# Performance work log

Measured on AMD Instinct MI355X. Metric: run time of the kernel, lower is better.

## Reference

```python
import jax, jax.numpy as jnp
from jax import lax
import numpy as np

K = 3          # k_size
STRIDE = 1
LAMDA = 10.0
B, H, W_, D = 2, 64, 64, 64


def extract_patches(x, k, stride, same):
    """TF tf.image.extract_patches layout: per-position vector ordered (ki, kj, channel)."""
    b, h, w, d = x.shape
    kn = (k - 1) // 2
    if same:  # SAME padding, stride 1 (as used for fg patches)
        x = jnp.pad(x, ((0, 0), (kn, kn), (kn, kn), (0, 0)))
        ph, pw = h, w
    else:     # VALID with stride
        ph = (h - k) // stride + 1
        pw = (w - k) // stride + 1
    cols = [x[:, i:i + (ph - 1) * stride + 1:stride, j:j + (pw - 1) * stride + 1:stride, :]
            for i in range(k) for j in range(k)]
    return jnp.stack(cols, axis=3).reshape(b, ph, pw, k * k * d)


def setup_inputs() -> dict:
    key = jax.random.key(0)
    k1, k2, k3, k4 = jax.random.split(key, 4)
    bg_in = jax.random.normal(k1, (B, H, W_, D), jnp.float32)
    fg_in = jax.random.normal(k2, (B, H, W_, D), jnp.float32)
    m = (jax.random.uniform(k3, (B, H, W_, 1)) > 0.3).astype(jnp.float32)
    mask = jnp.broadcast_to(m, (B, H, W_, D)) + jnp.zeros((), jnp.float32)
    W_ml = jax.random.normal(k4, (2 * D, D), jnp.float32) * 0.05  # 1x1 conv 'ML'
    b_ml = jnp.zeros((D,), jnp.float32)
    return {"bg_in": bg_in, "fg_in": fg_in, "mask": mask, "W_ml": W_ml, "b_ml": b_ml}


def reference(bg_in, fg_in, mask, W_ml, b_ml):
    b, h, w, d = bg_in.shape
    kn = (K - 1) // 2
    # nearest resize to (h,w) is identity here; take channel 0, tile to d channels
    mask_r = jnp.broadcast_to(mask[..., :1], (b, h, w, d))
    bg = bg_in * mask_r
    ph = (h - K) // STRIDE + 1
    pw = (w - K) // STRIDE + 1
    c = ph * pw
    # background patches: (b, c, k*k*d); foreground patches: (b, h, w, k*k*d)
    patch1 = extract_patches(bg, K, STRIDE, False).reshape(b, c, K * K * d)
    patch2 = extract_patches(fg_in, K, 1, True)
    k1d = jnp.sum(patch1 * patch1, axis=2)          # (b, c)
    wwd = jnp.sum(patch2 * patch2, axis=3)          # (b, h, w)
    # 1x1 conv of fg patches against bg patch bank == cross-correlation
    CS = jnp.einsum('bhwp,bcp->bhwc', patch2, patch1)
    DS1 = k1d[:, None, None, :] + wwd[..., None] - 2.0 * CS   # squared distances (b,h,w,c)
    mu = jnp.mean(DS1, axis=-1, keepdims=True)
    sd = jnp.std(DS1, axis=-1, keepdims=True)       # population std, as tf.math.reduce_std
    DS2 = -jnp.tanh((DS1 - mu) / sd)
    # exp(x-3)/sum(exp(x-3)) == softmax(x)
    CA = jax.nn.softmax(LAMDA * DS2, axis=-1)       # (b, h, w, c)
    # per-sample transposed conv with bg patches as kernel (k2: (b,K,K,d,c))
    k2 = patch1.reshape(b, c, K, K, d).transpose(0, 2, 3, 4, 1)
    # tf.nn.conv2d_transpose == gradient of SAME conv: correlate with rot180 kernel, swap I/O
    kt = k2[:, ::-1, ::-1].transpose(0, 1, 2, 4, 3)  # (b, K, K, c, d)

    def tconv(ca, ker):
        return lax.conv_general_dilated(ca[None], ker, (1, 1), 'SAME',
                                        dimension_numbers=('NHWC', 'HWIO', 'NHWC'))[0]

    ACL = jax.vmap(tconv)(CA, kt) / float(K * K)    # (b, h, w, d)
    ACL = bg + ACL * (1.0 - mask_r)
    con1 = jnp.concatenate([bg_in, ACL], axis=-1)   # (b, h, w, 2d)
    out = jax.nn.elu(jnp.einsum('bhwc,co->bhwo', con1, W_ml) + b_ml)
    return out
```

## Files before the change

kernel.cpp:

```cpp
#include <hip/hip_runtime.h>
#include <hip/hip_fp16.h>
#include <math.h>

#define BB 2
#define HH 64
#define WW 64
#define DD 64
#define PH 62
#define CC 3844
#define CCP 3968
#define PL 576
#define PLP 640
#define TP 8
#define LAM 10.0f

typedef _Float16 f16;
typedef __attribute__((ext_vector_type(8))) _Float16 half8;
typedef __attribute__((ext_vector_type(4))) float f32x4;

#define REQ_FAST 90030080ULL

__device__ __forceinline__ void gld16(const void* g, void* l) {
  __builtin_amdgcn_global_load_lds((const __attribute__((address_space(1))) void*)g,
                                   (__attribute__((address_space(3))) void*)l, 16, 0, 0);
}

__global__ __launch_bounds__(256) void k_prep2(
    const float* __restrict__ bg_in, const float* __restrict__ fg,
    const float* __restrict__ mask, float* __restrict__ bg,
    f16* __restrict__ bgf, f16* __restrict__ fgp) {
  const int NBG = BB * 4288 * 64;
  const int NFG = BB * 4356 * 64;
  int idx = blockIdx.x * 256 + threadIdx.x;
  if (idx < NBG) {
    int ch = idx & 63;
    int pix = (idx >> 6) % 4288;
    int b = idx / (4288 * 64);
    if (pix < 4096) {
      size_t src = ((size_t)b * 4096 + pix) * 64 + ch;
      float v = bg_in[src] * mask[((size_t)b * 4096 + pix) * 64];
      bg[src] = v;
      bgf[idx] = (f16)v;
    } else {
      bgf[idx] = (f16)0.f;
    }
  } else if (idx < NBG + NFG) {
    int i2 = idx - NBG;
    int ch = i2 & 63;
    int pix = (i2 >> 6) % 4356;
    int b = i2 / (4356 * 64);
    int yy = pix / 66, xx = pix - 66 * yy;
    float v = 0.f;
    if (yy >= 1 && yy <= 64 && xx >= 1 && xx <= 64)
      v = fg[(((size_t)b * 64 + (yy - 1)) * 64 + (xx - 1)) * 64 + ch];
    fgp[i2] = (f16)v;
  }
}

__global__ __launch_bounds__(256) void k_p1t(const float* __restrict__ bg,
                                             f16* __restrict__ P1T) {
  int idx = blockIdx.x * 256 + threadIdx.x;
  if (idx >= BB * PLP * CCP) return;
  int c = idx % CCP;
  int rest = idx / CCP;
  int r = rest % PLP, b = rest / PLP;
  float v = 0.f;
  if (r < PL && c < CC) {
    int ci = c / PH, cj = c - ci * PH;
    int kk = r >> 6, ch = r & 63;
    int ki = kk / 3, kj = kk - 3 * ki;
    v = bg[(((size_t)b * HH + ci + ki) * WW + cj + kj) * DD + ch];
  }
  P1T[idx] = (f16)v;
}

__global__ __launch_bounds__(256) void k_k1d2(const float* __restrict__ bg,
                                              float* __restrict__ k1d) {
  int idx = blockIdx.x * 256 + threadIdx.x;
  if (idx >= BB * CC) return;
  int b = idx / CC, c = idx - b * CC;
  int ci = c / PH, cj = c - ci * PH;
  float s = 0.f;
  for (int ki = 0; ki < 3; ++ki)
    for (int kj = 0; kj < 3; ++kj) {
      const float4* p =
          (const float4*)(bg + (((size_t)(b * HH + ci + ki) * WW) + cj + kj) * DD);
#pragma unroll
      for (int q = 0; q < 16; ++q) {
        float4 v = p[q];
        s += v.x * v.x + v.y * v.y + v.z * v.z + v.w * v.w;
      }
    }
  k1d[(size_t)b * CCP + c] = s;
}

__global__ __launch_bounds__(512) void k_gemm1(
    const f16* __restrict__ fgp, const f16* __restrict__ bgf,
    f16* __restrict__ CS) {
  __shared__ f16 tA[2][128 * 64];
  __shared__ f16 tB[2][128 * 64];
  const int tid = threadIdx.x;
  const int l = tid & 63, w = tid >> 6;
  const int b = blockIdx.z;
  const int m0 = blockIdx.y * 128, n0 = blockIdx.x * 128;
  const f16* fgB = fgp + (size_t)b * (4356 * 64);
  const f16* bgB = bgf + (size_t)b * (4288 * 64);

  int pixA[2], chSA[2], aCh[2];
#pragma unroll
  for (int i = 0; i < 2; ++i) {
    aCh[i] = w * 2 + i;
    int li = aCh[i] * 64 + l;
    int r = li >> 3;
    int j = (li & 7) ^ (r & 7);
    chSA[i] = j * 8;
    int pos = m0 + r;
    pixA[i] = (pos >> 6) * 66 + (pos & 63);
  }
  int pixB[2], chSB[2], bCh[2];
#pragma unroll
  for (int i = 0; i < 2; ++i) {
    bCh[i] = w * 2 + i;
    int li = bCh[i] * 64 + l;
    int r = li >> 3;
    int j = (li & 7) ^ (r & 7);
    chSB[i] = j * 8;
    int c = n0 + r;
    if (c < CC) {
      int ci = c / 62;
      pixB[i] = ci * 64 + (c - 62 * ci);
    } else {
      pixB[i] = 4096;
    }
  }

  const int wm = (w >> 2) * 64, wn = (w & 3) * 32;
  const int lr = l & 15, lk = l >> 4;
  const int xr = (lr & 7) << 4;

  f32x4 acc[4][2];
#pragma unroll
  for (int mi = 0; mi < 4; ++mi)
#pragma unroll
    for (int ni = 0; ni < 2; ++ni) acc[mi][ni] = (f32x4){0.f, 0.f, 0.f, 0.f};

#pragma unroll
  for (int i = 0; i < 2; ++i) {
    gld16(fgB + (size_t)pixA[i] * 64 + chSA[i], (char*)tA[0] + aCh[i] * 1024);
    gld16(bgB + (size_t)pixB[i] * 64 + chSB[i], (char*)tB[0] + bCh[i] * 1024);
  }
  asm volatile("s_waitcnt vmcnt(0)" ::: "memory");
  __syncthreads();

#pragma unroll 1
  for (int t = 0; t < 9; ++t) {
    const int cur = t & 1;
    if (t + 1 < 9) {
      const int tn = t + 1;
      const int ki = tn / 3, kj = tn - 3 * ki;
      const int offA = ki * 66 + kj, offB = ki * 64 + kj;
#pragma unroll
      for (int i = 0; i < 2; ++i) {
        gld16(fgB + (size_t)(pixA[i] + offA) * 64 + chSA[i],
              (char*)tA[cur ^ 1] + aCh[i] * 1024);
        gld16(bgB + (size_t)(pixB[i] + offB) * 64 + chSB[i],
              (char*)tB[cur ^ 1] + bCh[i] * 1024);
      }
    }
#pragma unroll
    for (int kk = 0; kk < 2; ++kk) {
      half8 av[4], bv[2];
      const int cb = lk * 16 + kk * 64;
#pragma unroll
      for (int mi = 0; mi < 4; ++mi) {
        int r = wm + mi * 16 + lr;
        av[mi] = *(const half8*)((const char*)tA[cur] + r * 128 + (cb ^ xr));
      }
#pragma unroll
      for (int ni = 0; ni < 2; ++ni) {
        int r = wn + ni * 16 + lr;
        bv[ni] = *(const half8*)((const char*)tB[cur] + r * 128 + (cb ^ xr));
      }
#pragma unroll
      for (int mi = 0; mi < 4; ++mi)
#pragma unroll
        for (int ni = 0; ni < 2; ++ni)
          acc[mi][ni] = __builtin_amdgcn_mfma_f32_16x16x32_f16(
              av[mi], bv[ni], acc[mi][ni], 0, 0, 0);
    }
    asm volatile("s_waitcnt vmcnt(0)" ::: "memory");
    __syncthreads();
  }

  CS += (size_t)b * 4096 * CCP;
#pragma unroll
  for (int mi = 0; mi < 4; ++mi) {
#pragma unroll
    for (int q = 0; q < 4; ++q) {
      int m = m0 + wm + mi * 16 + lk * 4 + q;
#pragma unroll
      for (int ni = 0; ni < 2; ++ni) {
        int n = n0 + wn + ni * 16 + lr;
        CS[(size_t)m * CCP + n] = (f16)acc[mi][ni][q];
      }
    }
  }
}

__global__ __launch_bounds__(512) void k_gemm2(
    const f16* __restrict__ A, const f16* __restrict__ B, f16* __restrict__ C,
    const float* __restrict__ sden) {
  __shared__ f16 tA[2][64 * 64];
  __shared__ f16 tB[2][128 * 64];
  const int tid = threadIdx.x;
  const int l = tid & 63, w = tid >> 6;
  const int p = blockIdx.x;
  const int L = (p & 7) * 80 + (p >> 3);
  const int b = L / 320;
  const int rL = L - b * 320;
  const int mt = rL / 5, nt = rL - mt * 5;
  const int m0 = mt * 64, n0 = nt * 128;
  A += (size_t)b * 4096 * CCP;
  B += (size_t)b * PLP * CCP;
  C += (size_t)b * 4096 * PLP;
  const float* sd = sden + (size_t)b * 4096;

  size_t aOff;
  {
    int li = w * 64 + l;
    int r = li >> 3;
    int j = (li & 7) ^ (r & 7);
    aOff = (size_t)(m0 + r) * CCP + j * 8;
  }
  size_t bOff[2];
  int bCh[2];
#pragma unroll
  for (int i = 0; i < 2; ++i) {
    bCh[i] = w * 2 + i;
    int li = bCh[i] * 64 + l;
    int r = li >> 3;
    int j = (li & 7) ^ (r & 7);
    bOff[i] = (size_t)(n0 + r) * CCP + j * 8;
  }

  const int wm = (w >> 2) * 32, wn = (w & 3) * 32;
  const int lr = l & 15, lk = l >> 4;
  const int xr = (lr & 7) << 4;

  f32x4 acc[2][2];
#pragma unroll
  for (int mi = 0; mi < 2; ++mi)
#pragma unroll
    for (int ni = 0; ni < 2; ++ni) acc[mi][ni] = (f32x4){0.f, 0.f, 0.f, 0.f};

  auto STAGE = [&](int buf, int k0) {
    gld16(A + aOff + k0, (char*)tA[buf] + w * 1024);
#pragma unroll
    for (int i = 0; i < 2; ++i)
      gld16(B + bOff[i] + k0, (char*)tB[buf] + bCh[i] * 1024);
  };

  const int NT = CCP / 64;
  STAGE(0, 0);
  asm volatile("s_waitcnt vmcnt(0)" ::: "memory");
  __syncthreads();

#pragma unroll 1
  for (int t = 0; t < NT; ++t) {
    const int cur = t & 1;
    if (t + 1 < NT) STAGE(cur ^ 1, (t + 1) * 64);
#pragma unroll
    for (int kk = 0; kk < 2; ++kk) {
      half8 av[2], bv[2];
      const int cb = lk * 16 + kk * 64;
#pragma unroll
      for (int mi = 0; mi < 2; ++mi) {
        int r = wm + mi * 16 + lr;
        av[mi] = *(const half8*)((const char*)tA[cur] + r * 128 + (cb ^ xr));
      }
#pragma unroll
      for (int ni = 0; ni < 2; ++ni) {
        int r = wn + ni * 16 + lr;
        bv[ni] = *(const half8*)((const char*)tB[cur] + r * 128 + (cb ^ xr));
      }
#pragma unroll
      for (int mi = 0; mi < 2; ++mi)
#pragma unroll
        for (int ni = 0; ni < 2; ++ni)
          acc[mi][ni] = __builtin_amdgcn_mfma_f32_16x16x32_f16(
              av[mi], bv[ni], acc[mi][ni], 0, 0, 0);
    }
    asm volatile("s_waitcnt vmcnt(0)" ::: "memory");
    __syncthreads();
  }

#pragma unroll
  for (int mi = 0; mi < 2; ++mi) {
#pragma unroll
    for (int q = 0; q < 4; ++q) {
      int m = m0 + wm + mi * 16 + lk * 4 + q;
      float sc = sd[m];
#pragma unroll
      for (int ni = 0; ni < 2; ++ni) {
        int n = n0 + wn + ni * 16 + lr;
        C[(size_t)m * PLP + n] = (f16)(acc[mi][ni][q] * sc);
      }
    }
  }
}

__global__ __launch_bounds__(256) void k_stats(f16* __restrict__ CS,
                                               const float* __restrict__ k1d,
                                               float* __restrict__ sden) {
  __shared__ float red[8];
  const int tid = threadIdx.x;
  const int row = blockIdx.x, b = blockIdx.y;
  f16* cs = CS + ((size_t)b * 4096 + row) * CCP;
  const float* kd = k1d + (size_t)b * CCP;
  const int base = tid * 16;
  const bool act = base < CCP;

  float tv[16];
  float s1 = 0.f, s2 = 0.f;
  if (act) {
    half8 v0 = ((const half8*)(cs + base))[0];
    half8 v1 = ((const half8*)(cs + base))[1];
    float kv[16];
    *(float4*)(kv + 0) = ((const float4*)(kd + base))[0];
    *(float4*)(kv + 4) = ((const float4*)(kd + base))[1];
    *(float4*)(kv + 8) = ((const float4*)(kd + base))[2];
    *(float4*)(kv + 12) = ((const float4*)(kd + base))[3];
#pragma unroll
    for (int i = 0; i < 16; ++i) {
      float cval = (float)(i < 8 ? v0[i] : v1[i - 8]);
      float t = (base + i < CC) ? (kv[i] - 2.f * cval) : 0.f;
      tv[i] = t;
      s1 += t;
      s2 = fmaf(t, t, s2);
    }
  } else {
#pragma unroll
    for (int i = 0; i < 16; ++i) tv[i] = 0.f;
  }
#pragma unroll
  for (int m = 32; m; m >>= 1) {
    s1 += __shfl_xor(s1, m, 64);
    s2 += __shfl_xor(s2, m, 64);
  }
  if ((tid & 63) == 0) {
    red[tid >> 6] = s1;
    red[4 + (tid >> 6)] = s2;
  }
  __syncthreads();
  float mu = (red[0] + red[1] + red[2] + red[3]) * (1.f / CC);
  float ex2 = (red[4] + red[5] + red[6] + red[7]) * (1.f / CC);
  float var = fmaxf(ex2 - mu * mu, 1e-12f);
  float rsd = rsqrtf(var);
  __syncthreads();

  float den = 0.f;
  if (act) {
    half8 w0, w1;
#pragma unroll
    for (int i = 0; i < 16; ++i) {
      float wv = 0.f;
      if (base + i < CC) {
        float z = (tv[i] - mu) * rsd;
        float e2z = __expf(2.f * z);
        float th = 1.f - 2.f / (e2z + 1.f);
        wv = __expf(-LAM * th);
        den += wv;
      }
      if (i < 8) w0[i] = (f16)wv; else w1[i - 8] = (f16)wv;
    }
    ((half8*)(cs + base))[0] = w0;
    ((half8*)(cs + base))[1] = w1;
  }
#pragma unroll
  for (int m = 32; m; m >>= 1) den += __shfl_xor(den, m, 64);
  if ((tid & 63) == 0) red[tid >> 6] = den;
  __syncthreads();
  if (tid == 0)
    sden[(size_t)b * 4096 + row] = 1.f / (9.f * (red[0] + red[1] + red[2] + red[3]));
}

__global__ __launch_bounds__(256) void k_final2(
    const float* __restrict__ bg_in, const float* __restrict__ mask,
    const float* __restrict__ bg, const f16* __restrict__ N2,
    const float* __restrict__ Wml, const float* __restrict__ bml,
    float* __restrict__ out) {
  __shared__ float s_con[4 * 128];
  const int tid = threadIdx.x;
  const int posg = blockIdx.x * 4;
  for (int i = tid; i < 4 * 128; i += 256) {
    int p = i >> 7, c = i & 127;
    int pos = posg + p;
    float v;
    if (c < 64) {
      v = bg_in[(size_t)pos * DD + c];
    } else {
      int cc = c - 64;
      int bwx = pos & 4095, bb = pos >> 12;
      int y = bwx >> 6, x = bwx & 63;
      float a = 0.f;
#pragma unroll
      for (int s = 0; s < 3; ++s) {
        int yy = y + 1 - s;
        if (yy < 0 || yy >= HH) continue;
#pragma unroll
        for (int t = 0; t < 3; ++t) {
          int xx = x + 1 - t;
          if (xx < 0 || xx >= WW) continue;
          a += (float)N2[((size_t)bb * 4096 + yy * 64 + xx) * PLP + (s * 3 + t) * 64 + cc];
        }
      }
      float m0 = mask[(size_t)pos * DD];
      v = bg[(size_t)pos * DD + cc] + a * (1.f - m0);
    }
    s_con[i] = v;
  }
  __syncthreads();
  const int o = tid & 63, p = tid >> 6;
  float sum = bml[o];
  const float* cp = s_con + (p << 7);
#pragma unroll 8
  for (int c = 0; c < 128; ++c) sum = fmaf(cp[c], Wml[c * 64 + o], sum);
  out[(size_t)(posg + p) * 64 + o] = (sum > 0.f) ? sum : expm1f(sum);
}

#define WS_BG    0
#define WS_BGT   524288
#define WS_K1D   1048576
#define WS_ACLN  1056264

__global__ __launch_bounds__(256) void k_prep(
    const float* __restrict__ bg_in, const float* __restrict__ mask,
    float* __restrict__ bg, float* __restrict__ bgT) {
  int idx = blockIdx.x * 256 + threadIdx.x;
  if (idx >= BB * HH * WW * DD) return;
  int ch = idx & 63, pos = idx >> 6;
  float m = mask[(size_t)pos * DD];
  float v = bg_in[idx] * m;
  bg[idx] = v;
  int x = pos & 63, rest = pos >> 6;
  int y = rest & 63, b = rest >> 6;
  bgT[(((size_t)b * DD + ch) * HH + y) * WW + x] = v;
}

__global__ __launch_bounds__(256) void k_k1d(const float* __restrict__ bg,
                                             float* __restrict__ k1d) {
  int idx = blockIdx.x * 256 + threadIdx.x;
  if (idx >= BB * CC) return;
  int b = idx / CC, c = idx - b * CC;
  int ci = c / PH, cj = c - ci * PH;
  float s = 0.f;
  for (int ki = 0; ki < 3; ++ki)
    for (int kj = 0; kj < 3; ++kj) {
      const float4* p =
          (const float4*)(bg + (((size_t)(b * HH + ci + ki) * WW) + cj + kj) * DD);
#pragma unroll
      for (int q = 0; q < 16; ++q) {
        float4 v = p[q];
        s += v.x * v.x + v.y * v.y + v.z * v.z + v.w * v.w;
      }
    }
  k1d[idx] = s;
}

__global__ __launch_bounds__(256, 2) void k_heavy(
    const float* __restrict__ fg, const float* __restrict__ bg,
    const float* __restrict__ bgT, const float* __restrict__ k1d,
    float* __restrict__ acln) {
  __shared__ _Float16 s_cs[TP * CC];
  __shared__ float s_fg[TP * PL];
  __shared__ float s_red[8];
  __shared__ float s_wwd[TP];
  __shared__ float s_den[TP];

  const int tid = threadIdx.x;
  const int X0 = blockIdx.x * TP;
  const int Y = blockIdx.y;
  const int b = blockIdx.z;

  for (int i = tid; i < TP * PL; i += 256) {
    int p = i / PL, r = i - p * PL;
    int kk = r >> 6, ch = r & 63;
    int ki = kk / 3, kj = kk - 3 * ki;
    int hy = Y + ki - 1, wx = X0 + p + kj - 1;
    float v = 0.f;
    if (hy >= 0 && hy < HH && wx >= 0 && wx < WW)
      v = fg[(((size_t)b * HH + hy) * WW + wx) * DD + ch];
    s_fg[i] = v;
  }
  __syncthreads();
  {
    int p = tid >> 5, lane = tid & 31;
    float a = 0.f;
    for (int r = lane; r < PL; r += 32) {
      float v = s_fg[p * PL + r];
      a = fmaf(v, v, a);
    }
#pragma unroll
    for (int m = 16; m; m >>= 1) a += __shfl_xor(a, m, 64);
    if (lane == 0) s_wwd[p] = a;
  }
  __syncthreads();

  const float* bgTb = bgT + (size_t)b * DD * HH * WW;
  for (int sw = 0; sw < 4; ++sw) {
    const int cb = sw * 256 + tid;
    float acc[TP][4];
#pragma unroll
    for (int p = 0; p < TP; ++p)
#pragma unroll
      for (int q = 0; q < 4; ++q) acc[p][q] = 0.f;
    int off4[4];
#pragma unroll
    for (int q = 0; q < 4; ++q) {
      int c = cb + q * 1024;
      if (c >= CC) c = CC - 1;
      int ci = c / PH;
      off4[q] = ci * WW + (c - ci * PH);
    }
    for (int ch = 0; ch < DD; ++ch) {
      const float* bgTc = bgTb + (size_t)ch * (HH * WW);
#pragma unroll
      for (int kk = 0; kk < 9; ++kk) {
        const int ki = kk / 3, kj = kk - 3 * (kk / 3);
        float fv[TP];
#pragma unroll
        for (int p = 0; p < TP; ++p) fv[p] = s_fg[p * PL + (kk << 6) + ch];
        float bv[4];
#pragma unroll
        for (int q = 0; q < 4; ++q) bv[q] = bgTc[off4[q] + ki * WW + kj];
#pragma unroll
        for (int p = 0; p < TP; ++p)
#pragma unroll
          for (int q = 0; q < 4; ++q) acc[p][q] = fmaf(fv[p], bv[q], acc[p][q]);
      }
    }
#pragma unroll
    for (int q = 0; q < 4; ++q) {
      int c = cb + q * 1024;
      if (c < CC) {
#pragma unroll
        for (int p = 0; p < TP; ++p) s_cs[p * CC + c] = (_Float16)acc[p][q];
      }
    }
  }
  __syncthreads();

  const float* k1db = k1d + b * CC;
  for (int pos = 0; pos < TP; ++pos) {
    __syncthreads();
    const float wwdp = s_wwd[pos];
    float s1 = 0.f, s2 = 0.f;
    for (int c = tid; c < CC; c += 256) {
      float ds1 = k1db[c] + wwdp - 2.f * (float)s_cs[pos * CC + c];
      s1 += ds1;
      s2 = fmaf(ds1, ds1, s2);
    }
#pragma unroll
    for (int m = 32; m; m >>= 1) {
      s1 += __shfl_xor(s1, m, 64);
      s2 += __shfl_xor(s2, m, 64);
    }
    if ((tid & 63) == 0) {
      int w = tid >> 6;
      s_red[w] = s1;
      s_red[4 + w] = s2;
    }
    __syncthreads();
    float mu = (s_red[0] + s_red[1] + s_red[2] + s_red[3]) * (1.f / CC);
    float ex2 = (s_red[4] + s_red[5] + s_red[6] + s_red[7]) * (1.f / CC);
    float var = fmaxf(ex2 - mu * mu, 1e-12f);
    float rsd = rsqrtf(var);
    float dp = 0.f;
    for (int c = tid; c < CC; c += 256) {
      float ds1 = k1db[c] + wwdp - 2.f * (float)s_cs[pos * CC + c];
      float z = (ds1 - mu) * rsd;
      float wv = expf(-LAM * tanhf(z));
      s_cs[pos * CC + c] = (_Float16)wv;
      dp += wv;
    }
#pragma unroll
    for (int m = 32; m; m >>= 1) dp += __shfl_xor(dp, m, 64);
    __syncthreads();
    if ((tid & 63) == 0) s_red[tid >> 6] = dp;
    __syncthreads();
    if (tid == 0) s_den[pos] = s_red[0] + s_red[1] + s_red[2] + s_red[3];
  }

  const int d = tid & 63;
  const int grp = tid >> 6;
  const int oA = grp, oB = grp + 4;
  const int sA = oA / 3, tA = oA - 3 * sA;
  const int sB = oB / 3, tB = oB - 3 * sB;
  const bool hasC = (grp == 0);
  const int offA = (sA * WW + tA) * DD + d;
  const int offB = (sB * WW + tB) * DD + d;
  const int offC = (2 * WW + 2) * DD + d;
  float aA[TP], aB[TP], aC[TP];
#pragma unroll
  for (int p = 0; p < TP; ++p) { aA[p] = 0.f; aB[p] = 0.f; aC[p] = 0.f; }
  const float* bgb = bg + (size_t)b * HH * WW * DD;
  float* s_wf = s_fg;
  int cj = 0, rowoff = 0;
  for (int c0 = 0; c0 < CC; c0 += 128) {
    const int n = (CC - c0 < 128) ? (CC - c0) : 128;
    __syncthreads();
    for (int i = tid; i < TP * 128; i += 256) {
      int p = i >> 7, cc = i & 127;
      s_wf[i] = (cc < n) ? (float)s_cs[p * CC + c0 + cc] : 0.f;
    }
    __syncthreads();
    for (int cc = 0; cc < n; cc += 2) {
      float2 wv[TP];
#pragma unroll
      for (int p = 0; p < TP; ++p)
        wv[p] = *(const float2*)(s_wf + (p << 7) + cc);
      {
        const float* rp = bgb + (size_t)rowoff * DD;
        float bA = rp[offA], bB = rp[offB], bCv = rp[offC];
#pragma unroll
        for (int p = 0; p < TP; ++p) {
          aA[p] = fmaf(wv[p].x, bA, aA[p]);
          aB[p] = fmaf(wv[p].x, bB, aB[p]);
          if (hasC) aC[p] = fmaf(wv[p].x, bCv, aC[p]);
        }
        ++rowoff;
        if (++cj == PH) { cj = 0; rowoff += 2; }
      }
      {
        const float* rp = bgb + (size_t)rowoff * DD;
        float bA = rp[offA], bB = rp[offB], bCv = rp[offC];
#pragma unroll
        for (int p = 0; p < TP; ++p) {
          aA[p] = fmaf(wv[p].y, bA, aA[p]);
          aB[p] = fmaf(wv[p].y, bB, aB[p]);
          if (hasC) aC[p] = fmaf(wv[p].y, bCv, aC[p]);
        }
        ++rowoff;
        if (++cj == PH) { cj = 0; rowoff += 2; }
      }
    }
  }
  __syncthreads();
#pragma unroll
  for (int p = 0; p < TP; ++p) {
    const float inv = 1.f / (9.f * s_den[p]);
    float* dst = acln + ((((size_t)b * HH + Y) * WW + (X0 + p)) * 9) * 64;
    dst[oA * 64 + d] = aA[p] * inv;
    dst[oB * 64 + d] = aB[p] * inv;
    if (hasC) dst[512 + d] = aC[p] * inv;
  }
}

__global__ __launch_bounds__(256) void k_final(
    const float* __restrict__ bg_in, const float* __restrict__ mask,
    const float* __restrict__ bg, const float* __restrict__ acln,
    const float* __restrict__ Wml, const float* __restrict__ bml,
    float* __restrict__ out) {
  __shared__ float s_con[4 * 128];
  const int tid = threadIdx.x;
  const int posg = blockIdx.x * 4;
  for (int i = tid; i < 4 * 128; i += 256) {
    int p = i >> 7, c = i & 127;
    int pos = posg + p;
    float v;
    if (c < 64) {
      v = bg_in[(size_t)pos * DD + c];
    } else {
      int cc = c - 64;
      int bwx = pos & 4095, bb = pos >> 12;
      int y = bwx >> 6, x = bwx & 63;
      float a = 0.f;
#pragma unroll
      for (int s = 0; s < 3; ++s) {
        int yy = y + 1 - s;
        if (yy < 0 || yy >= HH) continue;
#pragma unroll
        for (int t = 0; t < 3; ++t) {
          int xx = x + 1 - t;
          if (xx < 0 || xx >= WW) continue;
          a += acln[((((size_t)bb * HH + yy) * WW + xx) * 9 + (s * 3 + t)) * 64 + cc];
        }
      }
      float m0 = mask[(size_t)pos * DD];
      v = bg[(size_t)pos * DD + cc] + a * (1.f - m0);
    }
    s_con[i] = v;
  }
  __syncthreads();
  const int o = tid & 63, p = tid >> 6;
  float sum = bml[o];
  const float* cp = s_con + (p << 7);
#pragma unroll 8
  for (int c = 0; c < 128; ++c) sum = fmaf(cp[c], Wml[c * 64 + o], sum);
  out[(size_t)(posg + p) * 64 + o] = (sum > 0.f) ? sum : expm1f(sum);
}

extern "C" void kernel_launch(void* const* d_in, const int* in_sizes, int n_in,
                              void* d_out, int out_size, void* d_ws, size_t ws_size,
                              hipStream_t stream) {
  const float* bg_in = (const float*)d_in[0];
  const float* fg_in = (const float*)d_in[1];
  const float* mask = (const float*)d_in[2];
  const float* Wml = (const float*)d_in[3];
  const float* bml = (const float*)d_in[4];
  float* out = (float*)d_out;

  if (ws_size >= REQ_FAST) {
    char* w8 = (char*)d_ws;
    float* bg = (float*)(w8 + 0);
    f16* fgp = (f16*)(w8 + 2097152);
    f16* bgf = (f16*)(w8 + 3212288);
    f16* P1T = (f16*)(w8 + 4310016);
    f16* CS = (f16*)(w8 + 14468096);
    f16* N2 = (f16*)(w8 + 79479808);
    float* k1d = (float*)(w8 + 89965568);
    float* sden = (float*)(w8 + 89997312);

    const int NPREP = BB * 4288 * 64 + BB * 4356 * 64;
    k_prep2<<<dim3((NPREP + 255) / 256), dim3(256), 0, stream>>>(
        bg_in, fg_in, mask, bg, bgf, fgp);
    k_p1t<<<dim3((BB * PLP * CCP) / 256), dim3(256), 0, stream>>>(bg, P1T);
    k_k1d2<<<dim3((BB * CC + 255) / 256), dim3(256), 0, stream>>>(bg, k1d);
    k_gemm1<<<dim3(CCP / 128, 32, 2), dim3(512), 0, stream>>>(fgp, bgf, CS);
    k_stats<<<dim3(4096, 2), dim3(256), 0, stream>>>(CS, k1d, sden);
    k_gemm2<<<dim3(640), dim3(512), 0, stream>>>(CS, P1T, N2, sden);
    k_final2<<<dim3(2048), dim3(256), 0, stream>>>(bg_in, mask, bg, N2, Wml, bml, out);
  } else {
    float* ws = (float*)d_ws;
    float* bg = ws + WS_BG;
    float* bgT = ws + WS_BGT;
    float* k1d = ws + WS_K1D;
    float* acln = ws + WS_ACLN;
    k_prep<<<dim3(2048), dim3(256), 0, stream>>>(bg_in, mask, bg, bgT);
    k_k1d<<<dim3((BB * CC + 255) / 256), dim3(256), 0, stream>>>(bg, k1d);
    k_heavy<<<dim3(8, 64, 2), dim3(256), 0, stream>>>(fg_in, bg, bgT, k1d, acln);
    k_final<<<dim3(2048), dim3(256), 0, stream>>>(bg_in, mask, bg, acln, Wml, bml, out);
  }
}
```

Baseline: 195.6 us.

## Fuse prep kernels into one launch and triple-buffer gemm2 with priority hints

Merges the three preprocessing kernels (masked bg cast, P1T patch build, k1d norms) into a single launch. Each now reads bg_in*mask directly, so the fp32 bg buffer is no longer materialized, and the final kernel recomputes bg the same way. Separately, gemm2 moves from double to triple LDS buffering with a two-stage prefetch, a partial vmcnt wait, and s_setprio around the MFMA block to overlap loads with compute. The intent is fewer launches, less intermediate traffic and better latency hiding, at the cost of more LDS per block (possible occupancy drop) and redundant mask reads in the fused kernel.

```diff
diff --git a/kernel.cpp b/kernel.cpp
--- a/kernel.cpp
+++ b/kernel.cpp
@@ -25,25 +25,24 @@
                                    (__attribute__((address_space(3))) void*)l, 16, 0, 0);
 }
 
-__global__ __launch_bounds__(256) void k_prep2(
+__global__ __launch_bounds__(256) void k_preall(
     const float* __restrict__ bg_in, const float* __restrict__ fg,
-    const float* __restrict__ mask, float* __restrict__ bg,
-    f16* __restrict__ bgf, f16* __restrict__ fgp) {
+    const float* __restrict__ mask, f16* __restrict__ bgf,
+    f16* __restrict__ fgp, f16* __restrict__ P1T, float* __restrict__ k1d) {
   const int NBG = BB * 4288 * 64;
   const int NFG = BB * 4356 * 64;
+  const int NP1T = BB * PLP * CCP;
   int idx = blockIdx.x * 256 + threadIdx.x;
   if (idx < NBG) {
     int ch = idx & 63;
     int pix = (idx >> 6) % 4288;
     int b = idx / (4288 * 64);
+    f16 v = (f16)0.f;
     if (pix < 4096) {
       size_t src = ((size_t)b * 4096 + pix) * 64 + ch;
-      float v = bg_in[src] * mask[((size_t)b * 4096 + pix) * 64];
-      bg[src] = v;
-      bgf[idx] = (f16)v;
-    } else {
-      bgf[idx] = (f16)0.f;
-    }
+      v = (f16)(bg_in[src] * mask[((size_t)b * 4096 + pix) * 64]);
+    }
+    bgf[idx] = v;
   } else if (idx < NBG + NFG) {
     int i2 = idx - NBG;
     int ch = i2 & 63;
@@ -54,44 +53,40 @@
     if (yy >= 1 && yy <= 64 && xx >= 1 && xx <= 64)
       v = fg[(((size_t)b * 64 + (yy - 1)) * 64 + (xx - 1)) * 64 + ch];
     fgp[i2] = (f16)v;
-  }
-}
-
-__global__ __launch_bounds__(256) void k_p1t(const float* __restrict__ bg,
-                                             f16* __restrict__ P1T) {
-  int idx = blockIdx.x * 256 + threadIdx.x;
-  if (idx >= BB * PLP * CCP) return;
-  int c = idx % CCP;
-  int rest = idx / CCP;
-  int r = rest % PLP, b = rest / PLP;
-  float v = 0.f;
-  if (r < PL && c < CC) {
+  } else if (idx < NBG + NFG + NP1T) {
+    int i3 = idx - (NBG + NFG);
+    int c = i3 % CCP;
+    int rest = i3 / CCP;
+    int r = rest % PLP, b = rest / PLP;
+    float v = 0.f;
+    if (r < PL && c < CC) {
+      int ci = c / PH, cj = c - ci * PH;
+      int kk = r >> 6, ch = r & 63;
+      int ki = kk / 3, kj = kk - 3 * ki;
+      int pix = (ci + ki) * WW + cj + kj;
+      v = bg_in[((size_t)b * 4096 + pix) * 64 + ch] *
+          mask[((size_t)b * 4096 + pix) * 64];
+    }
+    P1T[i3] = (f16)v;
+  } else if (idx < NBG + NFG + NP1T + BB * CC) {
+    int i4 = idx - (NBG + NFG + NP1T);
+    int b = i4 / CC, c = i4 - b * CC;
     int ci = c / PH, cj = c - ci * PH;
-    int kk = r >> 6, ch = r & 63;
-    int ki = kk / 3, kj = kk - 3 * ki;
-    v = bg[(((size_t)b * HH + ci + ki) * WW + cj + kj) * DD + ch];
-  }
-  P1T[idx] = (f16)v;
-}
-
-__global__ __launch_bounds__(256) void k_k1d2(const float* __restrict__ bg,
-                                              float* __restrict__ k1d) {
-  int idx = blockIdx.x * 256 + threadIdx.x;
-  if (idx >= BB * CC) return;
-  int b = idx / CC, c = idx - b * CC;
-  int ci = c / PH, cj = c - ci * PH;
-  float s = 0.f;
-  for (int ki = 0; ki < 3; ++ki)
-    for (int kj = 0; kj < 3; ++kj) {
-      const float4* p =
-          (const float4*)(bg + (((size_t)(b * HH + ci + ki) * WW) + cj + kj) * DD);
-#pragma unroll
-      for (int q = 0; q < 16; ++q) {
-        float4 v = p[q];
-        s += v.x * v.x + v.y * v.y + v.z * v.z + v.w * v.w;
-      }
-    }
-  k1d[(size_t)b * CCP + c] = s;
+    float s = 0.f;
+    for (int ki = 0; ki < 3; ++ki)
+      for (int kj = 0; kj < 3; ++kj) {
+        int pix = (ci + ki) * WW + cj + kj;
+        float m = mask[((size_t)b * 4096 + pix) * 64];
+        float m2 = m * m;
+        const float4* p = (const float4*)(bg_in + ((size_t)b * 4096 + pix) * 64);
+#pragma unroll
+        for (int q = 0; q < 16; ++q) {
+          float4 v = p[q];
+          s += m2 * (v.x * v.x + v.y * v.y + v.z * v.z + v.w * v.w);
+        }
+      }
+    k1d[(size_t)b * CCP + c] = s;
+  }
 }
 
 __global__ __launch_bounds__(512) void k_gemm1(
@@ -210,8 +205,8 @@
 __global__ __launch_bounds__(512) void k_gemm2(
     const f16* __restrict__ A, const f16* __restrict__ B, f16* __restrict__ C,
     const float* __restrict__ sden) {
-  __shared__ f16 tA[2][64 * 64];
-  __shared__ f16 tB[2][128 * 64];
+  __shared__ f16 tA[3][64 * 64];
+  __shared__ f16 tB[3][128 * 64];
   const int tid = threadIdx.x;
   const int l = tid & 63, w = tid >> 6;
   const int p = blockIdx.x;
@@ -259,16 +254,8 @@
     for (int i = 0; i < 2; ++i)
       gld16(B + bOff[i] + k0, (char*)tB[buf] + bCh[i] * 1024);
   };
-
-  const int NT = CCP / 64;
-  STAGE(0, 0);
-  asm volatile("s_waitcnt vmcnt(0)" ::: "memory");
-  __syncthreads();
-
-#pragma unroll 1
-  for (int t = 0; t < NT; ++t) {
-    const int cur = t & 1;
-    if (t + 1 < NT) STAGE(cur ^ 1, (t + 1) * 64);
+  auto COMPUTE = [&](int buf) {
+    __builtin_amdgcn_s_setprio(1);
 #pragma unroll
     for (int kk = 0; kk < 2; ++kk) {
       half8 av[2], bv[2];
@@ -276,12 +263,12 @@
 #pragma unroll
       for (int mi = 0; mi < 2; ++mi) {
         int r = wm + mi * 16 + lr;
-        av[mi] = *(const half8*)((const char*)tA[cur] + r * 128 + (cb ^ xr));
+        av[mi] = *(const half8*)((const char*)tA[buf] + r * 128 + (cb ^ xr));
       }
 #pragma unroll
       for (int ni = 0; ni < 2; ++ni) {
         int r = wn + ni * 16 + lr;
-        bv[ni] = *(const half8*)((const char*)tB[cur] + r * 128 + (cb ^ xr));
+        bv[ni] = *(const half8*)((const char*)tB[buf] + r * 128 + (cb ^ xr));
       }
 #pragma unroll
       for (int mi = 0; mi < 2; ++mi)
@@ -290,9 +277,30 @@
           acc[mi][ni] = __builtin_amdgcn_mfma_f32_16x16x32_f16(
               av[mi], bv[ni], acc[mi][ni], 0, 0, 0);
     }
-    asm volatile("s_waitcnt vmcnt(0)" ::: "memory");
-    __syncthreads();
-  }
+    __builtin_amdgcn_s_setprio(0);
+  };
+
+  const int NT = CCP / 64;
+  STAGE(0, 0);
+  STAGE(1, 64);
+  int cur = 0, pre = 2, kpre = 128;
+#pragma unroll 1
+  for (int t = 0; t < NT - 2; ++t) {
+    asm volatile("s_waitcnt vmcnt(3)" ::: "memory");
+    __builtin_amdgcn_s_barrier();
+    STAGE(pre, kpre);
+    COMPUTE(cur);
+    cur = (cur == 2) ? 0 : cur + 1;
+    pre = (pre == 2) ? 0 : pre + 1;
+    kpre += 64;
+  }
+  asm volatile("s_waitcnt vmcnt(3)" ::: "memory");
+  __builtin_amdgcn_s_barrier();
+  COMPUTE(cur);
+  cur = (cur == 2) ? 0 : cur + 1;
+  asm volatile("s_waitcnt vmcnt(0)" ::: "memory");
+  __builtin_amdgcn_s_barrier();
+  COMPUTE(cur);
 
 #pragma unroll
   for (int mi = 0; mi < 2; ++mi) {
@@ -386,9 +394,8 @@
 
 __global__ __launch_bounds__(256) void k_final2(
     const float* __restrict__ bg_in, const float* __restrict__ mask,
-    const float* __restrict__ bg, const f16* __restrict__ N2,
-    const float* __restrict__ Wml, const float* __restrict__ bml,
-    float* __restrict__ out) {
+    const f16* __restrict__ N2, const float* __restrict__ Wml,
+    const float* __restrict__ bml, float* __restrict__ out) {
   __shared__ float s_con[4 * 128];
   const int tid = threadIdx.x;
   const int posg = blockIdx.x * 4;
@@ -415,7 +422,7 @@
         }
       }
       float m0 = mask[(size_t)pos * DD];
-      v = bg[(size_t)pos * DD + cc] + a * (1.f - m0);
+      v = bg_in[(size_t)pos * DD + cc] * m0 + a * (1.f - m0);
     }
     s_con[i] = v;
   }
@@ -712,7 +719,6 @@
 
   if (ws_size >= REQ_FAST) {
     char* w8 = (char*)d_ws;
-    float* bg = (float*)(w8 + 0);
     f16* fgp = (f16*)(w8 + 2097152);
     f16* bgf = (f16*)(w8 + 3212288);
     f16* P1T = (f16*)(w8 + 4310016);
@@ -721,15 +727,14 @@
     float* k1d = (float*)(w8 + 89965568);
     float* sden = (float*)(w8 + 89997312);
 
-    const int NPREP = BB * 4288 * 64 + BB * 4356 * 64;
-    k_prep2<<<dim3((NPREP + 255) / 256), dim3(256), 0, stream>>>(
-        bg_in, fg_in, mask, bg, bgf, fgp);
-    k_p1t<<<dim3((BB * PLP * CCP) / 256), dim3(256), 0, stream>>>(bg, P1T);
-    k_k1d2<<<dim3((BB * CC + 255) / 256), dim3(256), 0, stream>>>(bg, k1d);
+    const int NPREP =
+        BB * 4288 * 64 + BB * 4356 * 64 + BB * PLP * CCP + BB * CC;
+    k_preall<<<dim3((NPREP + 255) / 256), dim3(256), 0, stream>>>(
+        bg_in, fg_in, mask, bgf, fgp, P1T, k1d);
     k_gemm1<<<dim3(CCP / 128, 32, 2), dim3(512), 0, stream>>>(fgp, bgf, CS);
     k_stats<<<dim3(4096, 2), dim3(256), 0, stream>>>(CS, k1d, sden);
     k_gemm2<<<dim3(640), dim3(512), 0, stream>>>(CS, P1T, N2, sden);
-    k_final2<<<dim3(2048), dim3(256), 0, stream>>>(bg_in, mask, bg, N2, Wml, bml, out);
+    k_final2<<<dim3(2048), dim3(256), 0, stream>>>(bg_in, mask, N2, Wml, bml, out);
   } else {
     float* ws = (float*)d_ws;
     float* bg = ws + WS_BG;
```

Result: slower. 236.6 us (+20.9%).
